# Optimization experiments

Measured on AMD Instinct MI355X. Metric: run time of the kernel, lower is better.

## Reference

```python
import jax, jax.numpy as jnp
import numpy as np

TOKENS, IN_F, OUT_F = 8192, 4096, 4096


def setup_inputs() -> dict:
    key = jax.random.key(0)
    k1, k2 = jax.random.split(key)
    return {
        "input": jax.random.normal(k1, (TOKENS, IN_F), dtype=jnp.float32),
        "weight": jax.random.normal(k2, (OUT_F, IN_F), dtype=jnp.float32),
        "weight_scale": jnp.ones((1,), dtype=jnp.float32),
        "input_scale": jnp.ones((1,), dtype=jnp.float32),
    }


def reference(input, weight, weight_scale, input_scale):
    # BitNet-style: ternary weight quantization {-1, 0, +1} w.r.t. learned scale,
    # int8-range activation quantization, fused dequant-scaled matmul.
    ws = weight_scale[0]
    xs = input_scale[0]
    # quantize_weights: round(w / ws) clipped to ternary
    w_q = jnp.clip(jnp.round(weight / ws), -1.0, 1.0)          # [out, in], values in {-1,0,1}
    # fused_quantize_matmul: quantize activations to int8 range, matmul, dequant scale
    x_q = jnp.clip(jnp.round(input / xs), -128.0, 127.0)        # [tokens, in]
    out = jnp.einsum('ti,oi->to', x_q, w_q) * (xs * ws)         # [tokens, out]
    return out
```

## Files before the change

kernel.cpp:

```cpp
#include <hip/hip_runtime.h>
#include <stdint.h>


typedef int  int4v  __attribute__((ext_vector_type(4)));
typedef int  int16v __attribute__((ext_vector_type(16)));

typedef __attribute__((address_space(1))) void gvoid;
typedef __attribute__((address_space(3))) void lvoid;

#define M_DIM 8192
#define N_DIM 4096
#define K_DIM 4096

#define BM 256
#define BN 256
#define BK 128
#define NT (K_DIM / BK)

__global__ __launch_bounds__(256) void quant_kernel(
    const float* __restrict__ in, int8_t* __restrict__ out,
    const float* __restrict__ scale_ptr, float lo, float hi, long n) {
  long i = ((long)blockIdx.x * blockDim.x + threadIdx.x) * 16;
  if (i >= n) return;
  float s = scale_ptr[0];
  float4 a = *(const float4*)(in + i);
  float4 b = *(const float4*)(in + i + 4);
  float4 c = *(const float4*)(in + i + 8);
  float4 d = *(const float4*)(in + i + 12);
  float v[16] = {a.x, a.y, a.z, a.w, b.x, b.y, b.z, b.w,
                 c.x, c.y, c.z, c.w, d.x, d.y, d.z, d.w};
  union { int8_t c[16]; int4 q; } u;
#pragma unroll
  for (int t = 0; t < 16; ++t) {
    float q = rintf(v[t] / s);
    q = fminf(fmaxf(q, lo), hi);
    u.c[t] = (int8_t)q;
  }
  *(int4*)(out + i) = u.q;
}

__global__ __launch_bounds__(512, 2) void gemm_bt(
    const int8_t* __restrict__ A,
    const int8_t* __restrict__ B,
    float* __restrict__ C,
    const float* __restrict__ ws_ptr, const float* __restrict__ xs_ptr) {
  __shared__ __attribute__((aligned(16))) char smem[131072];

  const int tid  = threadIdx.x;
  const int wid  = tid >> 6;
  const int lane = tid & 63;
  const int wr   = wid >> 2;
  const int wc   = wid & 3;
  const int r    = lane & 31;
  const int half = lane >> 5;

  const int fl  = blockIdx.y * gridDim.x + blockIdx.x;
  const int vid = (fl & 7) * 64 + (fl >> 3);
  const long m0 = (long)(vid & 31) * BM;
  const long n0 = (long)(vid >> 5) * BN;

  const int srow   = wid * 8 + (lane >> 3);
  const int schunk = ((lane & 7) ^ (lane >> 3)) * 16;
  const int8_t* gA = A + (m0 + srow) * K_DIM + schunk;
  const int8_t* gB = B + (n0 + srow) * K_DIM + schunk;
  const int ldst = wid * 1024;

  int aRow[4], bRow[2], co[4];
#pragma unroll
  for (int m = 0; m < 4; ++m) aRow[m] = (wr * 128 + m * 32 + r) * BK;
#pragma unroll
  for (int n = 0; n < 2; ++n) bRow[n] = (wc * 64 + n * 32 + r) * BK;
#pragma unroll
  for (int ks = 0; ks < 4; ++ks) co[ks] = ((ks * 2 + half) ^ (r & 7)) * 16;

#define STAGE_A(kk, q, nb)                                                         \
  __builtin_amdgcn_global_load_lds(                                                \
      (gvoid*)(gA + (long)(kk) * BK + (long)(q) * 64 * K_DIM),                     \
      (lvoid*)(smem + (nb) * 32768 + (q) * 8192 + ldst), 16, 0, 0)
#define STAGE_B(kk, q, nb)                                                         \
  __builtin_amdgcn_global_load_lds(                                                \
      (gvoid*)(gB + (long)(kk) * BK + (long)(q) * 64 * K_DIM),                     \
      (lvoid*)(smem + 65536 + (nb) * 32768 + (q) * 8192 + ldst), 16, 0, 0)

  STAGE_A(0, 0, 0); STAGE_A(0, 2, 0);
  STAGE_B(0, 0, 0); STAGE_B(0, 1, 0); STAGE_B(0, 2, 0); STAGE_B(0, 3, 0);
  STAGE_A(0, 1, 0); STAGE_A(0, 3, 0);
  asm volatile("s_waitcnt vmcnt(2)" ::: "memory");
  __builtin_amdgcn_s_barrier();

  int4v  a[2][4], b0[4], b1[4];
  int16v acc[4][2] = {};

#pragma unroll 2
  for (int t = 0; t < NT; ++t) {
    const int bi = t & 1;
    const int nb = bi ^ 1;
    const char* sAb = smem + bi * 32768;
    const char* sBb = smem + 65536 + bi * 32768;
    int kk = t + 1; if (kk >= NT) kk = NT - 1;

#pragma unroll
    for (int m = 0; m < 2; ++m)
#pragma unroll
      for (int ks = 0; ks < 4; ++ks)
        a[m][ks] = *(const int4v*)(sAb + aRow[m] + co[ks]);
#pragma unroll
    for (int ks = 0; ks < 4; ++ks)
      b0[ks] = *(const int4v*)(sBb + bRow[0] + co[ks]);
    STAGE_A(kk, 0, nb); STAGE_A(kk, 2, nb);
    __builtin_amdgcn_s_barrier();
    __builtin_amdgcn_s_setprio(1);
#pragma unroll
    for (int ks = 0; ks < 4; ++ks) {
      acc[0][0] = __builtin_amdgcn_mfma_i32_32x32x32_i8(a[0][ks], b0[ks], acc[0][0], 0, 0, 0);
      acc[1][0] = __builtin_amdgcn_mfma_i32_32x32x32_i8(a[1][ks], b0[ks], acc[1][0], 0, 0, 0);
    }
    __builtin_amdgcn_s_setprio(0);
    __builtin_amdgcn_s_barrier();

#pragma unroll
    for (int ks = 0; ks < 4; ++ks)
      b1[ks] = *(const int4v*)(sBb + bRow[1] + co[ks]);
    STAGE_B(kk, 0, nb); STAGE_B(kk, 1, nb);
    asm volatile("s_waitcnt vmcnt(4)" ::: "memory");
    __builtin_amdgcn_s_barrier();
    __builtin_amdgcn_s_setprio(1);
#pragma unroll
    for (int ks = 0; ks < 4; ++ks) {
      acc[0][1] = __builtin_amdgcn_mfma_i32_32x32x32_i8(a[0][ks], b1[ks], acc[0][1], 0, 0, 0);
      acc[1][1] = __builtin_amdgcn_mfma_i32_32x32x32_i8(a[1][ks], b1[ks], acc[1][1], 0, 0, 0);
    }
    __builtin_amdgcn_s_setprio(0);
    __builtin_amdgcn_s_barrier();

#pragma unroll
    for (int m = 0; m < 2; ++m)
#pragma unroll
      for (int ks = 0; ks < 4; ++ks)
        a[m][ks] = *(const int4v*)(sAb + aRow[2 + m] + co[ks]);
    STAGE_B(kk, 2, nb); STAGE_B(kk, 3, nb);
    __builtin_amdgcn_s_barrier();
    __builtin_amdgcn_s_setprio(1);
#pragma unroll
    for (int ks = 0; ks < 4; ++ks) {
      acc[2][1] = __builtin_amdgcn_mfma_i32_32x32x32_i8(a[0][ks], b1[ks], acc[2][1], 0, 0, 0);
      acc[3][1] = __builtin_amdgcn_mfma_i32_32x32x32_i8(a[1][ks], b1[ks], acc[3][1], 0, 0, 0);
    }
    __builtin_amdgcn_s_setprio(0);
    __builtin_amdgcn_s_barrier();

    STAGE_A(kk, 1, nb); STAGE_A(kk, 3, nb);
    asm volatile("s_waitcnt vmcnt(2)" ::: "memory");
    __builtin_amdgcn_s_barrier();
    __builtin_amdgcn_s_setprio(1);
#pragma unroll
    for (int ks = 0; ks < 4; ++ks) {
      acc[2][0] = __builtin_amdgcn_mfma_i32_32x32x32_i8(a[0][ks], b0[ks], acc[2][0], 0, 0, 0);
      acc[3][0] = __builtin_amdgcn_mfma_i32_32x32x32_i8(a[1][ks], b0[ks], acc[3][0], 0, 0, 0);
    }
    __builtin_amdgcn_s_setprio(0);
    __builtin_amdgcn_s_barrier();
  }
  asm volatile("s_waitcnt vmcnt(0)" ::: "memory");

  const float s = ws_ptr[0] * xs_ptr[0];
#pragma unroll
  for (int m = 0; m < 4; ++m) {
#pragma unroll
    for (int n = 0; n < 2; ++n) {
      const long col = n0 + wc * 64 + n * 32 + r;
      const long rowbase = m0 + wr * 128 + m * 32 + 4 * half;
#pragma unroll
      for (int reg = 0; reg < 16; ++reg) {
        const long row = rowbase + (reg & 3) + 8 * (reg >> 2);
        C[row * N_DIM + col] = (float)acc[m][n][reg] * s;
      }
    }
  }
#undef STAGE_A
#undef STAGE_B
}

extern "C" void kernel_launch(void* const* d_in, const int* in_sizes, int n_in,
                              void* d_out, int out_size, void* d_ws, size_t ws_size,
                              hipStream_t stream) {
  const float* x  = (const float*)d_in[0];
  const float* w  = (const float*)d_in[1];
  const float* ws = (const float*)d_in[2];
  const float* xs = (const float*)d_in[3];
  float* out = (float*)d_out;

  int8_t* xq = (int8_t*)d_ws;
  int8_t* wq = (int8_t*)d_ws + (size_t)M_DIM * K_DIM;

  const long n_x = (long)M_DIM * K_DIM;
  const long n_w = (long)N_DIM * K_DIM;

  quant_kernel<<<(n_x / 16 + 255) / 256, 256, 0, stream>>>(x, xq, xs, -128.f, 127.f, n_x);
  quant_kernel<<<(n_w / 16 + 255) / 256, 256, 0, stream>>>(w, wq, ws, -1.f, 1.f, n_w);

  dim3 grid(N_DIM / BN, M_DIM / BM);
  gemm_bt<<<grid, 512, 0, stream>>>(xq, wq, out, ws, xs);
}
```

Before: 410.9 us.

## Fuse activation and weight quantization into one launch and drop trailing GEMM barriers

The two quantization launches are merged into a single kernel whose blocks branch on block index to handle either activations or weights. Each thread now processes two coalesced float4 chunks per block instead of sixteen contiguous floats, which removes one kernel launch and improves load coalescing. In the GEMM main loop, the barrier after each MFMA phase is removed, leaving one barrier per phase. This cuts synchronisation stalls but risks LDS hazards, since the next stage's global_load_lds writes may now race with other waves still reading the buffer.

Result: faster. 402.8 us (-2.0%).

```diff
diff --git a/kernel.cpp b/kernel.cpp
--- a/kernel.cpp
+++ b/kernel.cpp
@@ -17,26 +17,32 @@
 #define BK 128
 #define NT (K_DIM / BK)
 
-__global__ __launch_bounds__(256) void quant_kernel(
-    const float* __restrict__ in, int8_t* __restrict__ out,
-    const float* __restrict__ scale_ptr, float lo, float hi, long n) {
-  long i = ((long)blockIdx.x * blockDim.x + threadIdx.x) * 16;
-  if (i >= n) return;
-  float s = scale_ptr[0];
-  float4 a = *(const float4*)(in + i);
-  float4 b = *(const float4*)(in + i + 4);
-  float4 c = *(const float4*)(in + i + 8);
-  float4 d = *(const float4*)(in + i + 12);
-  float v[16] = {a.x, a.y, a.z, a.w, b.x, b.y, b.z, b.w,
-                 c.x, c.y, c.z, c.w, d.x, d.y, d.z, d.w};
-  union { int8_t c[16]; int4 q; } u;
-#pragma unroll
-  for (int t = 0; t < 16; ++t) {
-    float q = rintf(v[t] / s);
-    q = fminf(fmaxf(q, lo), hi);
-    u.c[t] = (int8_t)q;
+__global__ __launch_bounds__(256) void quant_fused(
+    const float* __restrict__ x, int8_t* __restrict__ xq,
+    const float* __restrict__ w, int8_t* __restrict__ wq,
+    const float* __restrict__ xs_ptr, const float* __restrict__ ws_ptr,
+    int nx_blocks) {
+  const bool isX = ((int)blockIdx.x < nx_blocks);
+  const float* __restrict__ in  = isX ? x : w;
+  int8_t* __restrict__ out      = isX ? xq : wq;
+  const float s  = isX ? xs_ptr[0] : ws_ptr[0];
+  const float lo = isX ? -128.f : -1.f;
+  const float hi = isX ?  127.f :  1.f;
+  const long base = (long)(isX ? blockIdx.x : (blockIdx.x - nx_blocks)) * 2048;
+#pragma unroll
+  for (int p = 0; p < 2; ++p) {
+    const long i = base + (long)p * 1024 + (long)threadIdx.x * 4;
+    float4 v = *(const float4*)(in + i);
+    float e[4] = {v.x, v.y, v.z, v.w};
+    union { int8_t c[4]; int u; } u;
+#pragma unroll
+    for (int t = 0; t < 4; ++t) {
+      float q = rintf(e[t] / s);
+      q = fminf(fmaxf(q, lo), hi);
+      u.c[t] = (int8_t)q;
+    }
+    *(int*)(out + i) = u.u;
   }
-  *(int4*)(out + i) = u.q;
 }
 
 __global__ __launch_bounds__(512, 2) void gemm_bt(
@@ -116,7 +122,6 @@
       acc[1][0] = __builtin_amdgcn_mfma_i32_32x32x32_i8(a[1][ks], b0[ks], acc[1][0], 0, 0, 0);
     }
     __builtin_amdgcn_s_setprio(0);
-    __builtin_amdgcn_s_barrier();
 
 #pragma unroll
     for (int ks = 0; ks < 4; ++ks)
@@ -131,7 +136,6 @@
       acc[1][1] = __builtin_amdgcn_mfma_i32_32x32x32_i8(a[1][ks], b1[ks], acc[1][1], 0, 0, 0);
     }
     __builtin_amdgcn_s_setprio(0);
-    __builtin_amdgcn_s_barrier();
 
 #pragma unroll
     for (int m = 0; m < 2; ++m)
@@ -147,7 +151,6 @@
       acc[3][1] = __builtin_amdgcn_mfma_i32_32x32x32_i8(a[1][ks], b1[ks], acc[3][1], 0, 0, 0);
     }
     __builtin_amdgcn_s_setprio(0);
-    __builtin_amdgcn_s_barrier();
 
     STAGE_A(kk, 1, nb); STAGE_A(kk, 3, nb);
     asm volatile("s_waitcnt vmcnt(2)" ::: "memory");
@@ -159,7 +162,6 @@
       acc[3][0] = __builtin_amdgcn_mfma_i32_32x32x32_i8(a[1][ks], b0[ks], acc[3][0], 0, 0, 0);
     }
     __builtin_amdgcn_s_setprio(0);
-    __builtin_amdgcn_s_barrier();
   }
   asm volatile("s_waitcnt vmcnt(0)" ::: "memory");
 
@@ -193,11 +195,9 @@
   int8_t* xq = (int8_t*)d_ws;
   int8_t* wq = (int8_t*)d_ws + (size_t)M_DIM * K_DIM;
 
-  const long n_x = (long)M_DIM * K_DIM;
-  const long n_w = (long)N_DIM * K_DIM;
-
-  quant_kernel<<<(n_x / 16 + 255) / 256, 256, 0, stream>>>(x, xq, xs, -128.f, 127.f, n_x);
-  quant_kernel<<<(n_w / 16 + 255) / 256, 256, 0, stream>>>(w, wq, ws, -1.f, 1.f, n_w);
+  const int nx_blocks = (int)((long)M_DIM * K_DIM / 2048);
+  const int nw_blocks = (int)((long)N_DIM * K_DIM / 2048);
+  quant_fused<<<nx_blocks + nw_blocks, 256, 0, stream>>>(x, xq, w, wq, xs, ws, nx_blocks);
 
   dim3 grid(N_DIM / BN, M_DIM / BM);
   gemm_bt<<<grid, 512, 0, stream>>>(xq, wq, out, ws, xs);
```
